# Optimization experiments

Measured on AMD Instinct MI355X. Metric: run time of the kernel, lower is better.

Reference implementation:

```python
import jax, jax.numpy as jnp
import numpy as np

H = W = 128
C = 256
NC = 15
BASE_SIZE = 8.0
SCALE = 4.0
RING = np.array([0, 1, 2, 5, 8, 7, 6, 3])  # clockwise ring of 3x3 kernel (row-major idx)
BIAS_CLS = float(-np.log((1.0 - 0.01) / 0.01))  # bias_init_with_prob(0.01)


def conv(x, w, b, pad):
    y = jax.lax.conv_general_dilated(x, w, (1, 1), [(pad, pad), (pad, pad)],
                                     dimension_numbers=('NCHW', 'OIHW', 'NCHW'))
    return y + b[None, :, None, None]


def conv_relu(x, w, b):
    return jax.nn.relu(conv(x, w, b, 1))


def gen_grid_anchors(h, w, stride):
    # AnchorGeneratorRotated: base anchor centered at 0.5*(base_size-1), shifted by stride grid
    ctr = 0.5 * (BASE_SIZE - 1.0)
    gx = jnp.arange(w, dtype=jnp.float32) * stride
    gy = jnp.arange(h, dtype=jnp.float32) * stride
    yy, xx = jnp.meshgrid(gy, gx, indexing='ij')  # row-major (y outer, x inner)
    size = BASE_SIZE * SCALE
    return jnp.stack([xx + ctr, yy + ctr,
                      jnp.full_like(xx, size), jnp.full_like(xx, size),
                      jnp.zeros_like(xx)], axis=-1).reshape(-1, 5)


def norm_angle(a):
    PI = np.pi
    return ((a + PI / 4.0) % PI) - PI / 4.0  # into [-pi/4, 3pi/4)


def rboxes_decode(anchors, deltas, wh_ratio_clip=1e-6):
    # anchors [HW,5], deltas [N,HW,5] -> [N,HW,5]
    max_ratio = float(np.abs(np.log(wh_ratio_clip)))
    dx, dy, dw, dh, dt = [deltas[..., i] for i in range(5)]
    dw = jnp.clip(dw, -max_ratio, max_ratio)
    dh = jnp.clip(dh, -max_ratio, max_ratio)
    ax, ay, aw, ah, aa = [anchors[..., i] for i in range(5)]
    cos, sin = jnp.cos(aa), jnp.sin(aa)
    gx = dx * aw * cos - dy * ah * sin + ax
    gy = dx * aw * sin + dy * ah * cos + ay
    gw = aw * jnp.exp(dw)
    gh = ah * jnp.exp(dh)
    ga = norm_angle(aa + dt)
    return jnp.stack([gx, gy, gw, gh, ga], axis=-1)


def bilinear_sample(x, ys, xs):
    # x [N,C,H,W]; ys/xs [N,H,W,K] float pixel coords -> [N,C,H,W,K], zero outside
    N, Cc, h, w = x.shape
    K = ys.shape[-1]
    x0 = jnp.floor(xs)
    y0 = jnp.floor(ys)
    wx1 = xs - x0
    wx0 = 1.0 - wx1
    wy1 = ys - y0
    wy0 = 1.0 - wy1
    xf = x.reshape(N, Cc, h * w)

    def gather(yi, wy, xi, wxx):
        valid = (yi >= 0) & (yi < h) & (xi >= 0) & (xi < w)
        yc = jnp.clip(yi, 0, h - 1).astype(jnp.int32)
        xc = jnp.clip(xi, 0, w - 1).astype(jnp.int32)
        idx = (yc * w + xc).reshape(N, -1)  # [N,H*W*K]
        v = jax.vmap(lambda xi_, ii_: jnp.take(xi_, ii_, axis=1))(xf, idx)
        v = v.reshape(N, Cc, h, w, K)
        wgt = jnp.where(valid, wy * wxx, 0.0)[:, None]  # [N,1,H,W,K]
        return v * wgt

    out = gather(y0, wy0, x0, wx0)
    out = out + gather(y0, wy0, x0 + 1.0, wx1)
    out = out + gather(y0 + 1.0, wy1, x0, wx0)
    out = out + gather(y0 + 1.0, wy1, x0 + 1.0, wx1)
    return out


def align_conv(x, refine_anchor, stride, w, b):
    # deformable 3x3 conv; sampling grid from refined rotated anchors
    N, Cc, h, ww = x.shape
    k = 3
    idx = jnp.arange(-1, 2, dtype=x.dtype)
    yy, xx = jnp.meshgrid(idx, idx, indexing='ij')
    xx = xx.reshape(-1)
    yy = yy.reshape(-1)  # [9] kernel offsets, row-major matching OIHW flatten
    axc, ayc, aw, ah, aa = [refine_anchor[..., i] for i in range(5)]
    s = jnp.asarray(stride, x.dtype)
    axc, ayc, aw, ah = axc / s, ayc / s, aw / s, ah / s
    cos, sin = jnp.cos(aa), jnp.sin(aa)
    dx = (aw / k)[..., None] * xx  # [N,h,w,9]
    dy = (ah / k)[..., None] * yy
    xs = cos[..., None] * dx - sin[..., None] * dy + axc[..., None]
    ys = sin[..., None] * dx + cos[..., None] * dy + ayc[..., None]
    sampled = bilinear_sample(x, ys, xs)  # [N,C,h,w,9]
    out = jnp.einsum('nchwk,ock->nohw', sampled, w.reshape(w.shape[0], Cc, 9))
    return jax.nn.relu(out + b[None, :, None, None])


def or_conv(x, w, b):
    # ORConv2d(256->32, arf_config=(1,8)): 8 spatially-rotated copies of each 3x3 filter
    o, ci = w.shape[0], w.shape[1]
    wf = w.reshape(o, ci, 9)
    rotated = []
    for r in range(8):
        src = np.arange(9)
        for j in range(8):
            src[RING[j]] = RING[(j - r) % 8]  # rotate ring by r*45deg, center fixed
        rotated.append(wf[..., src])
    wr = jnp.stack(rotated, axis=1).reshape(o * 8, ci, 3, 3)  # channel = o*8 + r
    br = jnp.repeat(b, 8)
    return conv(x, wr, br, 1)


def setup_inputs() -> dict:
    key = jax.random.key(0)
    ks = iter(jax.random.split(key, 32))
    d = {}
    d['feats'] = jax.random.normal(next(ks), (1, C, H, W), dtype=jnp.float32)
    def wlike(shape):
        return 0.01 * jax.random.normal(next(ks), shape, dtype=jnp.float32)
    d['fam_reg_w0'] = wlike((C, C, 3, 3)); d['fam_reg_b0'] = jnp.zeros((C,), jnp.float32)
    d['fam_reg_w1'] = wlike((C, C, 3, 3)); d['fam_reg_b1'] = jnp.zeros((C,), jnp.float32)
    d['fam_reg_hw'] = wlike((5, C, 1, 1)); d['fam_reg_hb'] = jnp.zeros((5,), jnp.float32)
    d['fam_cls_w0'] = wlike((C, C, 3, 3)); d['fam_cls_b0'] = jnp.zeros((C,), jnp.float32)
    d['fam_cls_w1'] = wlike((C, C, 3, 3)); d['fam_cls_b1'] = jnp.zeros((C,), jnp.float32)
    d['fam_cls_hw'] = wlike((NC, C, 1, 1)); d['fam_cls_hb'] = jnp.full((NC,), BIAS_CLS, jnp.float32)
    d['align_w'] = wlike((C, C, 3, 3)); d['align_b'] = jnp.zeros((C,), jnp.float32)
    d['or_w'] = wlike((C // 8, C, 3, 3)); d['or_b'] = jnp.zeros((C // 8,), jnp.float32)
    d['odm_reg_w0'] = wlike((C, C, 3, 3)); d['odm_reg_b0'] = jnp.zeros((C,), jnp.float32)
    d['odm_reg_w1'] = wlike((C, C, 3, 3)); d['odm_reg_b1'] = jnp.zeros((C,), jnp.float32)
    d['odm_reg_hw'] = wlike((5, C, 3, 3)); d['odm_reg_hb'] = jnp.zeros((5,), jnp.float32)
    d['odm_cls_w0'] = wlike((C, C // 8, 3, 3)); d['odm_cls_b0'] = jnp.zeros((C,), jnp.float32)
    d['odm_cls_w1'] = wlike((C, C, 3, 3)); d['odm_cls_b1'] = jnp.zeros((C,), jnp.float32)
    d['odm_cls_hw'] = wlike((NC, C, 3, 3)); d['odm_cls_hb'] = jnp.full((NC,), BIAS_CLS, jnp.float32)
    d['stride'] = 8
    return d


def reference(feats, fam_reg_w0, fam_reg_b0, fam_reg_w1, fam_reg_b1, fam_reg_hw, fam_reg_hb,
              fam_cls_w0, fam_cls_b0, fam_cls_w1, fam_cls_b1, fam_cls_hw, fam_cls_hb,
              align_w, align_b, or_w, or_b,
              odm_reg_w0, odm_reg_b0, odm_reg_w1, odm_reg_b1, odm_reg_hw, odm_reg_hb,
              odm_cls_w0, odm_cls_b0, odm_cls_w1, odm_cls_b1, odm_cls_hw, odm_cls_hb,
              stride):
    x = feats
    t = conv_relu(conv_relu(x, fam_reg_w0, fam_reg_b0), fam_reg_w1, fam_reg_b1)
    fam_bbox_pred = conv(t, fam_reg_hw, fam_reg_hb, 0)  # [N,5,h,w]
    t = conv_relu(conv_relu(x, fam_cls_w0, fam_cls_b0), fam_cls_w1, fam_cls_b1)
    fam_cls_pred = conv(t, fam_cls_hw, fam_cls_hb, 0)   # [N,NC,h,w]
    N, _, h, w = fam_bbox_pred.shape
    anchors = gen_grid_anchors(h, w, stride)  # [h*w,5]
    deltas = jax.lax.stop_gradient(fam_bbox_pred).transpose(0, 2, 3, 1).reshape(N, -1, 5)
    refine_anchor = rboxes_decode(anchors, deltas).reshape(N, h, w, 5)
    al = align_conv(x, refine_anchor, stride, align_w, align_b)  # [N,256,h,w]
    orf = or_conv(al, or_w, or_b)                                # [N,256,h,w]
    pooled = orf.reshape(N, -1, 8, h, w).max(axis=2)             # rotation-invariant pooling -> [N,32,h,w]
    t = conv_relu(conv_relu(pooled, odm_cls_w0, odm_cls_b0), odm_cls_w1, odm_cls_b1)
    odm_cls_pred = conv(t, odm_cls_hw, odm_cls_hb, 1)
    t = conv_relu(conv_relu(orf, odm_reg_w0, odm_reg_b0), odm_reg_w1, odm_reg_b1)
    odm_bbox_pred = conv(t, odm_reg_hw, odm_reg_hb, 1)
    return (fam_cls_pred, fam_bbox_pred, odm_cls_pred, odm_bbox_pred, anchors, refine_anchor)
```

## Files before the change

### kernel.cpp

```cpp
#include <hip/hip_runtime.h>
#include <hip/hip_bf16.h>
#include <hip/hip_fp16.h>

#define HW 128
#define NPX 16384
#define CC 256

typedef short  bf16x8  __attribute__((ext_vector_type(8)));
typedef short  short4v __attribute__((ext_vector_type(4)));
typedef float  f32x4   __attribute__((ext_vector_type(4)));
typedef unsigned int u32x4 __attribute__((ext_vector_type(4)));

static __device__ __forceinline__ short f2bs(float v) {
    union { float f; unsigned u; } x; x.f = v;
    unsigned r = x.u + 0x7FFFu + ((x.u >> 16) & 1u);
    return (short)(r >> 16);
}
static __device__ __forceinline__ float bs2f(short s) {
    union { unsigned u; float f; } x; x.u = ((unsigned)(unsigned short)s) << 16;
    return x.f;
}

static __device__ __forceinline__ int bx_swz() {
    return ((blockIdx.x & 7) << 5) | (blockIdx.x >> 3);
}

struct F8 { unsigned char b; };
__device__ __forceinline__ unsigned char enc8(float v) {
    unsigned short u = __half_as_ushort(__float2half(v));
    unsigned short s = u & 0x8000, mag = u & 0x7FFF;
    mag = (unsigned short)(mag + 0x0080);
    return (unsigned char)((unsigned short)(s | mag) >> 8);
}
__device__ __forceinline__ float dec8(F8 v) {
    return __half2float(__ushort_as_half((unsigned short)(v.b) << 8));
}
__device__ __forceinline__ float ldg_(const float* p) { return *p; }
__device__ __forceinline__ float ldg_(const F8* p)    { return dec8(*p); }

__constant__ int c_ROT9[8][9] = {
    {0,1,2,3,4,5,6,7,8},
    {3,0,1,6,4,2,7,8,5},
    {6,3,0,7,4,1,8,5,2},
    {7,6,3,8,4,0,5,2,1},
    {8,7,6,5,4,3,2,1,0},
    {5,8,7,2,4,6,1,0,3},
    {2,5,8,1,4,7,0,3,6},
    {1,2,5,0,4,8,3,6,7},
};

__device__ __forceinline__ void v9_decode_px(
    const float* bbox, int px, float s,
    float& gx, float& gy, float& gw, float& gh, float& ga)
{
    int y = px >> 7, x = px & 127;
    float ax = x * s + 3.5f, ay = y * s + 3.5f;
    float dx = bbox[0 * NPX + px];
    float dy = bbox[1 * NPX + px];
    float dw = bbox[2 * NPX + px];
    float dh = bbox[3 * NPX + px];
    float dt = bbox[4 * NPX + px];
    const float maxr = 13.815510558f;
    dw = fminf(fmaxf(dw, -maxr), maxr);
    dh = fminf(fmaxf(dh, -maxr), maxr);
    gx = dx * 32.f + ax;
    gy = dy * 32.f + ay;
    gw = 32.f * expf(dw);
    gh = 32.f * expf(dh);
    const float PI = 3.14159265358979323846f;
    float m = fmodf(dt + PI * 0.25f, PI);
    if (m < 0.f) m += PI;
    ga = m - PI * 0.25f;
}


__global__ __launch_bounds__(256) void v10_transpose(
    const float* __restrict__ f, short* __restrict__ xt)
{
    __shared__ float tile[32][33];
    int px0 = blockIdx.x * 32, ci0 = blockIdx.y * 32;
    int tx = threadIdx.x & 31, ty = threadIdx.x >> 5;
#pragma unroll
    for (int i = 0; i < 4; ++i) {
        int ci = ty + i * 8;
        tile[ci][tx] = f[(size_t)(ci0 + ci) * NPX + px0 + tx];
    }
    __syncthreads();
#pragma unroll
    for (int i = 0; i < 4; ++i) {
        int pxr = ty + i * 8;
        xt[(size_t)(px0 + pxr) * 256 + ci0 + tx] = f2bs(tile[tx][pxr]);
    }
}

__global__ __launch_bounds__(256) void v10_prep(
    const float* __restrict__ w, const float* __restrict__ bias,
    short* __restrict__ wb, float* __restrict__ bb,
    int Cout, int Cin, int OCP, int mode)
{
    int g = blockIdx.x * 256 + threadIdx.x;
    if (g < OCP) bb[g] = (g < Cout) ? ((mode == 1) ? bias[g >> 3] : bias[g]) : 0.f;
    int tot = 9 * OCP * Cin;
    if (g >= tot) return;
    int t   = g / (OCP * Cin);
    int rem = g - t * OCP * Cin;
    int oc  = rem / Cin;
    int ci  = rem - oc * Cin;
    float v = 0.f;
    if (oc < Cout) {
        if (mode == 0)      v = w[((size_t)oc * Cin + ci) * 9 + t];
        else if (mode == 1) { int o = oc >> 3, r = oc & 7;
                              v = w[((size_t)o * Cin + ci) * 9 + c_ROT9[r][t]]; }
        else if (t == 4)    v = w[(size_t)oc * Cin + ci];
    }
    wb[g] = f2bs(v);
}

__constant__ int c_JOB[14][5] = {
    {0,       256, 256, 256, 0},
    {589824,  256, 256, 256, 0},
    {1179648, 256, 256, 256, 0},
    {1769472, 256, 256, 256, 0},
    {2359296, 256, 256, 256, 0},
    {2949120, 256, 256, 256, 1},
    {3538944, 256, 256, 256, 0},
    {4128768, 256, 256, 256, 0},
    {4718592, 256, 256, 256, 0},
    {5308416, 5,   256, 64,  2},
    {5455872, 15,  256, 64,  2},
    {5603328, 5,   256, 64,  0},
    {5750784, 15,  256, 64,  0},
    {5898240, 256, 32,  256, 0},
};

__global__ __launch_bounds__(256) void v12_prepall(
    const float* w0, const float* w1, const float* w2, const float* w3,
    const float* w4, const float* w5, const float* w6, const float* w7,
    const float* w8, const float* w9, const float* w10, const float* w11,
    const float* w12, const float* w13,
    const float* b0, const float* b1, const float* b2, const float* b3,
    const float* b4, const float* b5, const float* b6, const float* b7,
    const float* b8, const float* b9, const float* b10, const float* b11,
    const float* b12, const float* b13,
    short* __restrict__ wball, float* __restrict__ bball)
{
    const float* ws_[14] = {w0,w1,w2,w3,w4,w5,w6,w7,w8,w9,w10,w11,w12,w13};
    const float* bs_[14] = {b0,b1,b2,b3,b4,b5,b6,b7,b8,b9,b10,b11,b12,b13};
    const int j = blockIdx.y;
    const int dst  = c_JOB[j][0];
    const int Cout = c_JOB[j][1];
    const int Cin  = c_JOB[j][2];
    const int OCP  = c_JOB[j][3];
    const int mode = c_JOB[j][4];
    const float* w = ws_[j];
    const float* bias = bs_[j];
    int g = blockIdx.x * 256 + threadIdx.x;
    if (g < OCP) bball[j * 256 + g] = (g < Cout) ? ((mode == 1) ? bias[g >> 3] : bias[g]) : 0.f;
    int tot = 9 * OCP * Cin;
    if (g >= tot) return;
    int t   = g / (OCP * Cin);
    int rem = g - t * OCP * Cin;
    int oc  = rem / Cin;
    int ci  = rem - oc * Cin;
    float v = 0.f;
    if (oc < Cout) {
        if (mode == 0)      v = w[((size_t)oc * Cin + ci) * 9 + t];
        else if (mode == 1) { int o = oc >> 3, r = oc & 7;
                              v = w[((size_t)o * Cin + ci) * 9 + c_ROT9[r][t]]; }
        else if (t == 4)    v = w[(size_t)oc * Cin + ci];
    }
    wball[dst + g] = f2bs(v);
}

template <int RELU, int HEAD, int ONLY1, int CIN, int OCG>
__device__ __forceinline__ void conv_body(
    short* S,
    const short* __restrict__ xin, const short* __restrict__ wb,
    const float* __restrict__ bb, void* __restrict__ outv,
    int CoutAct, int OCP, int bx, int oy)
{
    const int y    = bx >> 1;
    const int xh   = (bx & 1) * 64;
    const int ocb  = oy * 64 * OCG;
    const int tid  = threadIdx.x;
    const int wv   = tid >> 6;
    const int lane = tid & 63;
    const int quad = lane >> 4;
    const int l15  = lane & 15;
    const int ocw  = ocb + wv * 16 * OCG;

    int gofs[4], lofs[4];
#pragma unroll
    for (int i = 0; i < 4; ++i) {
        int e = tid + i * 256;
        gofs[i] = -1; lofs[i] = -1;
        if (e < 792) {
            int pos = e >> 2, part = e & 3;
            int r = pos / 66, c = pos - r * 66;
            int yy = y - 1 + r, xx = xh - 1 + c;
            lofs[i] = (r * 66 + c) * 40 + part * 8;
            if (yy >= 0 && yy < HW && xx >= 0 && xx < HW)
                gofs[i] = (yy * HW + xx) * CIN + part * 8;
        }
    }
    const bf16x8 zf = (bf16x8){0, 0, 0, 0, 0, 0, 0, 0};

    f32x4 acc[4][OCG];
#pragma unroll
    for (int p = 0; p < 4; ++p)
#pragma unroll
        for (int g = 0; g < OCG; ++g) acc[p][g] = (f32x4){0.f, 0.f, 0.f, 0.f};

    {
        bf16x8 st[4];
#pragma unroll
        for (int i = 0; i < 4; ++i) {
            st[i] = zf;
            if (gofs[i] >= 0) st[i] = *(const bf16x8*)(xin + gofs[i]);
        }
#pragma unroll
        for (int i = 0; i < 4; ++i)
            if (lofs[i] >= 0) *(bf16x8*)(&S[lofs[i]]) = st[i];
    }
    bf16x8 a[9][OCG];
#pragma unroll
    for (int t = (ONLY1 ? 4 : 0); t < (ONLY1 ? 5 : 9); ++t)
#pragma unroll
        for (int g = 0; g < OCG; ++g)
            a[t][g] = *(const bf16x8*)(wb +
                ((size_t)(t * OCP + ocw + g * 16 + l15) * CIN + quad * 8));
    __syncthreads();

    const int NST = CIN / 32;
    int cur = 0;
    for (int s = 0; s < NST; ++s) {
        const int cib = s * 32;

        bf16x8 st[4];
        if (s + 1 < NST) {
#pragma unroll
            for (int i = 0; i < 4; ++i) {
                st[i] = zf;
                if (gofs[i] >= 0)
                    st[i] = *(const bf16x8*)(xin + gofs[i] + cib + 32);
            }
        }

#pragma unroll
        for (int t = (ONLY1 ? 4 : 0); t < (ONLY1 ? 5 : 9); ++t) {
            const int r = t / 3, dxk = t % 3 - 1;
#pragma unroll
            for (int p = 0; p < 4; ++p) {
                int c = 1 + p * 16 + l15 + dxk;
                bf16x8 b = *(const bf16x8*)(&S[cur * 7920 + (r * 66 + c) * 40 + quad * 8]);
#pragma unroll
                for (int g = 0; g < OCG; ++g)
                    acc[p][g] = __builtin_amdgcn_mfma_f32_16x16x32_bf16(a[t][g], b, acc[p][g], 0, 0, 0);
            }
            if (s + 1 < NST) {
#pragma unroll
                for (int g = 0; g < OCG; ++g)
                    a[t][g] = *(const bf16x8*)(wb +
                        ((size_t)(t * OCP + ocw + g * 16 + l15) * CIN + cib + 32 + quad * 8));
            }
        }

        if (s + 1 < NST) {
#pragma unroll
            for (int i = 0; i < 4; ++i)
                if (lofs[i] >= 0) *(bf16x8*)(&S[(cur ^ 1) * 7920 + lofs[i]]) = st[i];
        }
        __syncthreads();
        cur ^= 1;
    }

#pragma unroll
    for (int p = 0; p < 4; ++p) {
        const int px = y * HW + xh + p * 16 + l15;
#pragma unroll
        for (int g = 0; g < OCG; ++g) {
            const int ocq = ocw + g * 16 + quad * 4;
            if (HEAD) {
                float* o = (float*)outv;
#pragma unroll
                for (int r = 0; r < 4; ++r)
                    if (ocq + r < CoutAct)
                        o[(size_t)(ocq + r) * NPX + px] = acc[p][g][r] + bb[ocq + r];
            } else {
                short4v s4;
#pragma unroll
                for (int r = 0; r < 4; ++r) {
                    float v = acc[p][g][r] + bb[ocq + r];
                    if (RELU) v = fmaxf(v, 0.f);
                    s4[r] = f2bs(v);
                }
                *(short4v*)((short*)outv + (size_t)px * 256 + ocq) = s4;
            }
        }
    }
}

template <int RELU, int HEAD, int ONLY1, int CIN, int OCG>
__global__ __launch_bounds__(256) void v13_conv(
    const short* __restrict__ xin, const short* __restrict__ wb,
    const float* __restrict__ bb, void* __restrict__ outv,
    int CoutAct, int OCP)
{
    __shared__ short S[2 * 7920];
    conv_body<RELU, HEAD, ONLY1, CIN, OCG>(S, xin, wb, bb, outv,
                                           CoutAct, OCP, bx_swz(), blockIdx.y);
}

template <int RELU, int HEAD, int ONLY1, int CIN0, int CIN1, int OCG, int NY, int OCP>
__global__ __launch_bounds__(256) void v13_pair(
    const short* __restrict__ in0, const short* __restrict__ in1,
    const short* __restrict__ wb0, const short* __restrict__ wb1,
    const float* __restrict__ bb0, const float* __restrict__ bb1,
    void* __restrict__ out0, void* __restrict__ out1,
    int cout0, int cout1)
{
    __shared__ short S[2 * 7920];
    const int ybr = blockIdx.y;
    if (ybr < NY)
        conv_body<RELU, HEAD, ONLY1, CIN0, OCG>(S, in0, wb0, bb0, out0,
                                                cout0, OCP, bx_swz(), ybr);
    else
        conv_body<RELU, HEAD, ONLY1, CIN1, OCG>(S, in1, wb1, bb1, out1,
                                                cout1, OCP, bx_swz(), ybr - NY);
}

__global__ __launch_bounds__(256) void v13_align(
    const short* __restrict__ xt, const float* __restrict__ bbox,
    const short* __restrict__ wb, const float* __restrict__ bb,
    const int* __restrict__ stride_p, short* __restrict__ outa)
{
    const int bx   = bx_swz();
    const int y    = bx >> 1;
    const int xh   = (bx & 1) * 64;
    const int ocb  = blockIdx.y * 128;
    const int tid  = threadIdx.x;
    const int wv   = tid >> 6, lane = tid & 63, quad = lane >> 4, l15 = lane & 15;
    const int ocw  = ocb + wv * 32;

    __shared__ int   s_idx[4][576];
    __shared__ float s_wgt[4][576];
    __shared__ short S[2][64 * 40];

    const float s = (float)(*stride_p);
    for (int e = tid; e < 576; e += 256) {
        int t = e >> 6, xi = e & 63;
        int px = y * HW + xh + xi;
        float gx, gy, gw, gh, ga;
        v9_decode_px(bbox, px, s, gx, gy, gw, gh, ga);
        float axc = gx / s, ayc = gy / s;
        float aw3 = gw / (3.f * s), ah3 = gh / (3.f * s);
        float cs = cosf(ga), sn = sinf(ga);
        float kx = (float)(t % 3 - 1), ky = (float)(t / 3 - 1);
        float ddx = aw3 * kx, ddy = ah3 * ky;
        float xf = cs * ddx - sn * ddy + axc;
        float yf = sn * ddx + cs * ddy + ayc;
        float fx = floorf(xf), fy = floorf(yf);
        int ix = (int)fx, iy = (int)fy;
        float wx1 = xf - fx, wx0 = 1.f - wx1;
        float wy1 = yf - fy, wy0 = 1.f - wy1;
        bool x0v = (ix >= 0) && (ix < HW), x1v = (ix + 1 >= 0) && (ix + 1 < HW);
        bool y0v = (iy >= 0) && (iy < HW), y1v = (iy + 1 >= 0) && (iy + 1 < HW);
        int x0c = min(max(ix, 0), HW - 1), x1c = min(max(ix + 1, 0), HW - 1);
        int y0c = min(max(iy, 0), HW - 1), y1c = min(max(iy + 1, 0), HW - 1);
        s_idx[0][e] = y0c * HW + x0c;
        s_idx[1][e] = y0c * HW + x1c;
        s_idx[2][e] = y1c * HW + x0c;
        s_idx[3][e] = y1c * HW + x1c;
        s_wgt[0][e] = (y0v && x0v) ? wy0 * wx0 : 0.f;
        s_wgt[1][e] = (y0v && x1v) ? wy0 * wx1 : 0.f;
        s_wgt[2][e] = (y1v && x0v) ? wy1 * wx0 : 0.f;
        s_wgt[3][e] = (y1v && x1v) ? wy1 * wx1 : 0.f;
    }

    f32x4 acc[4][2];
#pragma unroll
    for (int p = 0; p < 4; ++p) { acc[p][0] = (f32x4){0,0,0,0}; acc[p][1] = (f32x4){0,0,0,0}; }

    const int spx = tid >> 2;
    const int sq  = tid & 3;
    const int sw  = spx * 40 + sq * 8;
    const bf16x8 zf = (bf16x8){0, 0, 0, 0, 0, 0, 0, 0};

    __syncthreads();

    bf16x8 aC0, aC1;
    bf16x8 gN0, gN1, gN2, gN3;
    float  wN0, wN1, wN2, wN3;
    {
        int e = spx;
        int i0 = s_idx[0][e], i1 = s_idx[1][e], i2 = s_idx[2][e], i3 = s_idx[3][e];
        float w0 = s_wgt[0][e], w1 = s_wgt[1][e], w2 = s_wgt[2][e], w3 = s_wgt[3][e];
        const short* base = xt + sq * 8;
        bf16x8 g0 = *(const bf16x8*)(base + (size_t)i0 * 256);
        bf16x8 g1 = *(const bf16x8*)(base + (size_t)i1 * 256);
        bf16x8 g2 = *(const bf16x8*)(base + (size_t)i2 * 256);
        bf16x8 g3 = *(const bf16x8*)(base + (size_t)i3 * 256);
        float v[8];
#pragma unroll
        for (int i = 0; i < 8; ++i)
            v[i] = w0 * bs2f(g0[i]) + w1 * bs2f(g1[i]) + w2 * bs2f(g2[i]) + w3 * bs2f(g3[i]);
        u32x4 r;
#pragma unroll
        for (int i = 0; i < 4; ++i)
            asm("v_cvt_pk_bf16_f32 %0, %1, %2" : "=v"(r[i]) : "v"(v[2 * i]), "v"(v[2 * i + 1]));
        *(u32x4*)(&S[0][sw]) = r;
    }
    {
        int e = 64 + spx;
        int i0 = s_idx[0][e], i1 = s_idx[1][e], i2 = s_idx[2][e], i3 = s_idx[3][e];
        wN0 = s_wgt[0][e]; wN1 = s_wgt[1][e]; wN2 = s_wgt[2][e]; wN3 = s_wgt[3][e];
        const short* base = xt + sq * 8;
        gN0 = *(const bf16x8*)(base + (size_t)i0 * 256);
        gN1 = *(const bf16x8*)(base + (size_t)i1 * 256);
        gN2 = *(const bf16x8*)(base + (size_t)i2 * 256);
        gN3 = *(const bf16x8*)(base + (size_t)i3 * 256);
    }
    aC0 = *(const bf16x8*)(wb + ((size_t)(ocw + l15) * 256 + quad * 8));
    aC1 = *(const bf16x8*)(wb + ((size_t)(ocw + 16 + l15) * 256 + quad * 8));
    __syncthreads();

    int cur = 0;
    for (int cib = 0; cib < 256; cib += 32) {
        for (int t = 0; t < 9; ++t) {
            const bool have1 = !(cib == 224 && t == 8);
            const bool have2 = !(cib == 224 && t >= 7);
            const int t1 = (t == 8) ? 0 : t + 1;
            const int c1 = (t == 8) ? cib + 32 : cib;
            int t2 = t + 2, c2 = cib;
            if (t2 > 8) { t2 -= 9; c2 += 32; }

            bf16x8 gF0 = zf, gF1 = zf, gF2 = zf, gF3 = zf;
            float  wF0 = 0.f, wF1 = 0.f, wF2 = 0.f, wF3 = 0.f;
            if (have2) {
                int e = t2 * 64 + spx;
                int i0 = s_idx[0][e], i1 = s_idx[1][e], i2 = s_idx[2][e], i3 = s_idx[3][e];
                wF0 = s_wgt[0][e]; wF1 = s_wgt[1][e]; wF2 = s_wgt[2][e]; wF3 = s_wgt[3][e];
                const short* base = xt + c2 + sq * 8;
                gF0 = *(const bf16x8*)(base + (size_t)i0 * 256);
                gF1 = *(const bf16x8*)(base + (size_t)i1 * 256);
                gF2 = *(const bf16x8*)(base + (size_t)i2 * 256);
                gF3 = *(const bf16x8*)(base + (size_t)i3 * 256);
            }
            bf16x8 aN0 = aC0, aN1 = aC1;
            if (have1) {
                aN0 = *(const bf16x8*)(wb + ((size_t)(t1 * 256 + ocw + l15) * 256 + c1 + quad * 8));
                aN1 = *(const bf16x8*)(wb + ((size_t)(t1 * 256 + ocw + 16 + l15) * 256 + c1 + quad * 8));
            }

#pragma unroll
            for (int p = 0; p < 4; ++p) {
                bf16x8 b = *(const bf16x8*)(&S[cur][(p * 16 + l15) * 40 + quad * 8]);
                acc[p][0] = __builtin_amdgcn_mfma_f32_16x16x32_bf16(aC0, b, acc[p][0], 0, 0, 0);
                acc[p][1] = __builtin_amdgcn_mfma_f32_16x16x32_bf16(aC1, b, acc[p][1], 0, 0, 0);
            }

            if (have1) {
                float v[8];
#pragma unroll
                for (int i = 0; i < 8; ++i)
                    v[i] = wN0 * bs2f(gN0[i]) + wN1 * bs2f(gN1[i])
                         + wN2 * bs2f(gN2[i]) + wN3 * bs2f(gN3[i]);
                u32x4 r;
#pragma unroll
                for (int i = 0; i < 4; ++i)
                    asm("v_cvt_pk_bf16_f32 %0, %1, %2" : "=v"(r[i]) : "v"(v[2 * i]), "v"(v[2 * i + 1]));
                *(u32x4*)(&S[cur ^ 1][sw]) = r;
            }
            gN0 = gF0; gN1 = gF1; gN2 = gF2; gN3 = gF3;
            wN0 = wF0; wN1 = wF1; wN2 = wF2; wN3 = wF3;
            aC0 = aN0; aC1 = aN1;
            cur ^= 1;
            __syncthreads();
        }
    }

#pragma unroll
    for (int p = 0; p < 4; ++p) {
        const int px = y * HW + xh + p * 16 + l15;
#pragma unroll
        for (int g = 0; g < 2; ++g) {
            const int ocq = ocw + g * 16 + quad * 4;
            short4v s4;
#pragma unroll
            for (int r = 0; r < 4; ++r)
                s4[r] = f2bs(fmaxf(acc[p][g][r] + bb[ocq + r], 0.f));
            *(short4v*)(outa + (size_t)px * 256 + ocq) = s4;
        }
    }
}

__global__ __launch_bounds__(256) void v10_pool(
    const short* __restrict__ t1, short* __restrict__ p)
{
    int g = blockIdx.x * 256 + threadIdx.x;
    if (g >= 32 * NPX) return;
    int px = g >> 5, c = g & 31;
    const short* q = t1 + (size_t)px * 256 + c * 8;
    float m = bs2f(q[0]);
#pragma unroll
    for (int r = 1; r < 8; ++r) m = fmaxf(m, bs2f(q[r]));
    p[(size_t)px * 32 + c] = f2bs(m);
}

__global__ __launch_bounds__(256) void v9_decode(
    const float* __restrict__ bbox, float* __restrict__ anchors_out,
    float* __restrict__ refine_out, const int* __restrict__ stride_p)
{
    int px = blockIdx.x * 256 + threadIdx.x;
    if (px >= NPX) return;
    float s = (float)(*stride_p);
    int y = px >> 7, x = px & 127;
    anchors_out[px * 5 + 0] = x * s + 3.5f;
    anchors_out[px * 5 + 1] = y * s + 3.5f;
    anchors_out[px * 5 + 2] = 32.f;
    anchors_out[px * 5 + 3] = 32.f;
    anchors_out[px * 5 + 4] = 0.f;
    float gx, gy, gw, gh, ga;
    v9_decode_px(bbox, px, s, gx, gy, gw, gh, ga);
    refine_out[px * 5 + 0] = gx;
    refine_out[px * 5 + 1] = gy;
    refine_out[px * 5 + 2] = gw;
    refine_out[px * 5 + 3] = gh;
    refine_out[px * 5 + 4] = ga;
}

template <typename TIN, int RELU, int ORCONV>
__global__ __launch_bounds__(256) void v9_conv3x3(
    const TIN* __restrict__ in, const float* __restrict__ w,
    const float* __restrict__ bias, F8* __restrict__ out, int Cin)
{
    const int y   = blockIdx.x;
    const int ocb = blockIdx.y * 64;
    const int tid = threadIdx.x;
    const int xg  = tid & 15;
    const int og  = tid >> 4;
    const int x0  = xg * 8;
    const int oc0 = ocb + og * 4;

    __shared__ float srow[3][132];
    float acc[4][8];
#pragma unroll
    for (int i = 0; i < 4; ++i)
#pragma unroll
        for (int j = 0; j < 8; ++j) acc[i][j] = 0.f;

    for (int ci = 0; ci < Cin; ++ci) {
        __syncthreads();
        const TIN* inp = in + (size_t)ci * NPX;
        for (int t = tid; t < 3 * 130; t += 256) {
            int r = t / 130, c = t - r * 130;
            int yy = y - 1 + r, xx = c - 1;
            float v = 0.f;
            if (yy >= 0 && yy < HW && xx >= 0 && xx < HW) v = ldg_(inp + yy * HW + xx);
            srow[r][c] = v;
        }
        __syncthreads();
        float wv[4][9];
#pragma unroll
        for (int i = 0; i < 4; ++i) {
            if (ORCONV) {
                int oc = oc0 + i;
                const float* wp = w + ((size_t)(oc >> 3) * Cin + ci) * 9;
                const int* rot = c_ROT9[oc & 7];
#pragma unroll
                for (int k = 0; k < 9; ++k) wv[i][k] = wp[rot[k]];
            } else {
                const float* wp = w + ((size_t)(oc0 + i) * Cin + ci) * 9;
#pragma unroll
                for (int k = 0; k < 9; ++k) wv[i][k] = wp[k];
            }
        }
#pragma unroll
        for (int r = 0; r < 3; ++r) {
            float iv[10];
#pragma unroll
            for (int c = 0; c < 10; ++c) iv[c] = srow[r][x0 + c];
#pragma unroll
            for (int dxk = 0; dxk < 3; ++dxk)
#pragma unroll
                for (int i = 0; i < 4; ++i)
#pragma unroll
                    for (int j = 0; j < 8; ++j)
                        acc[i][j] += iv[j + dxk] * wv[i][r * 3 + dxk];
        }
    }
#pragma unroll
    for (int i = 0; i < 4; ++i) {
        float b = ORCONV ? bias[(oc0 + i) >> 3] : bias[oc0 + i];
#pragma unroll
        for (int j = 0; j < 8; ++j) {
            float v = acc[i][j] + b;
            if (RELU) v = fmaxf(v, 0.f);
            out[(size_t)(oc0 + i) * NPX + y * HW + x0 + j].b = enc8(v);
        }
    }
}

__global__ __launch_bounds__(256) void v9_head1x1(
    const F8* __restrict__ in, const float* __restrict__ w,
    const float* __restrict__ bias, float* __restrict__ out, int Cout)
{
    int g = blockIdx.x * 256 + threadIdx.x;
    if (g >= Cout * NPX) return;
    int px = g & (NPX - 1);
    int oc = g >> 14;
    float acc = bias[oc];
    const float* wp = w + (size_t)oc * CC;
    for (int ci = 0; ci < CC; ++ci)
        acc += dec8(in[(size_t)ci * NPX + px]) * wp[ci];
    out[g] = acc;
}

__global__ __launch_bounds__(256) void v9_head3x3(
    const F8* __restrict__ in, const float* __restrict__ w,
    const float* __restrict__ bias, float* __restrict__ out, int Cout)
{
    int g = blockIdx.x * 256 + threadIdx.x;
    if (g >= Cout * NPX) return;
    int px = g & (NPX - 1);
    int oc = g >> 14;
    int y = px >> 7, x = px & 127;
    float acc = bias[oc];
    for (int ci = 0; ci < CC; ++ci) {
        const F8* ip = in + (size_t)ci * NPX;
        const float* wp = w + ((size_t)oc * CC + ci) * 9;
#pragma unroll
        for (int dy = 0; dy < 3; ++dy) {
            int yy = y + dy - 1;
            if (yy < 0 || yy >= HW) continue;
#pragma unroll
            for (int dxk = 0; dxk < 3; ++dxk) {
                int xx = x + dxk - 1;
                if (xx < 0 || xx >= HW) continue;
                acc += dec8(ip[yy * HW + xx]) * wp[dy * 3 + dxk];
            }
        }
    }
    out[g] = acc;
}

__global__ __launch_bounds__(256) void v9_align(
    const float* __restrict__ in, const float* __restrict__ bbox,
    const float* __restrict__ w, const float* __restrict__ bias,
    const int* __restrict__ stride_p, F8* __restrict__ out)
{
    const int y   = blockIdx.x;
    const int ocb = blockIdx.y * 64;
    const int tid = threadIdx.x;
    const int xg  = tid & 15;
    const int og  = tid >> 4;
    const int x0  = xg * 8;
    const int oc0 = ocb + og * 4;

    __shared__ float smp[9][128];
    __shared__ int   s_ix[1152], s_iy[1152];
    __shared__ float s_wx1[1152], s_wy1[1152];

    const float s = (float)(*stride_p);
    for (int t = tid; t < 1152; t += 256) {
        int k = t >> 7, xx = t & 127;
        int px = y * HW + xx;
        float gx, gy, gw, gh, ga;
        v9_decode_px(bbox, px, s, gx, gy, gw, gh, ga);
        float axc = gx / s, ayc = gy / s;
        float aw3 = gw / (s * 3.f), ah3 = gh / (s * 3.f);
        float cs = cosf(ga), sn = sinf(ga);
        float kx = (float)(k % 3 - 1), ky = (float)(k / 3 - 1);
        float ddx = aw3 * kx, ddy = ah3 * ky;
        float xf = cs * ddx - sn * ddy + axc;
        float yf = sn * ddx + cs * ddy + ayc;
        float fx = floorf(xf), fy = floorf(yf);
        s_ix[t]  = (int)fx;
        s_iy[t]  = (int)fy;
        s_wx1[t] = xf - fx;
        s_wy1[t] = yf - fy;
    }

    float acc[4][8];
#pragma unroll
    for (int i = 0; i < 4; ++i)
#pragma unroll
        for (int j = 0; j < 8; ++j) acc[i][j] = 0.f;

    for (int ci = 0; ci < CC; ++ci) {
        __syncthreads();
        const float* ip = in + (size_t)ci * NPX;
        for (int t = tid; t < 1152; t += 256) {
            int ix = s_ix[t], iy = s_iy[t];
            float wx1 = s_wx1[t], wx0 = 1.f - wx1;
            float wy1 = s_wy1[t], wy0 = 1.f - wy1;
            float v = 0.f;
            bool xv0 = (ix >= 0) && (ix < HW);
            bool xv1 = (ix + 1 >= 0) && (ix + 1 < HW);
            bool yv0 = (iy >= 0) && (iy < HW);
            bool yv1 = (iy + 1 >= 0) && (iy + 1 < HW);
            if (yv0 && xv0) v += ip[iy * HW + ix] * wy0 * wx0;
            if (yv0 && xv1) v += ip[iy * HW + ix + 1] * wy0 * wx1;
            if (yv1 && xv0) v += ip[(iy + 1) * HW + ix] * wy1 * wx0;
            if (yv1 && xv1) v += ip[(iy + 1) * HW + ix + 1] * wy1 * wx1;
            smp[t >> 7][t & 127] = v;
        }
        __syncthreads();

        float wv[4][9];
#pragma unroll
        for (int i = 0; i < 4; ++i) {
            const float* wp = w + ((size_t)(oc0 + i) * CC + ci) * 9;
#pragma unroll
            for (int k = 0; k < 9; ++k) wv[i][k] = wp[k];
        }
#pragma unroll
        for (int k = 0; k < 9; ++k) {
            float iv[8];
#pragma unroll
            for (int j = 0; j < 8; ++j) iv[j] = smp[k][x0 + j];
#pragma unroll
            for (int i = 0; i < 4; ++i)
#pragma unroll
                for (int j = 0; j < 8; ++j)
                    acc[i][j] += iv[j] * wv[i][k];
        }
    }
#pragma unroll
    for (int i = 0; i < 4; ++i) {
        float b = bias[oc0 + i];
#pragma unroll
        for (int j = 0; j < 8; ++j)
            out[(size_t)(oc0 + i) * NPX + y * HW + x0 + j].b =
                enc8(fmaxf(acc[i][j] + b, 0.f));
    }
}

__global__ __launch_bounds__(256) void v9_pool(
    const F8* __restrict__ orf, F8* __restrict__ pooled)
{
    int g = blockIdx.x * 256 + threadIdx.x;
    if (g >= 32 * NPX) return;
    int px = g & (NPX - 1);
    int c  = g >> 14;
    float m = -3.4e38f;
#pragma unroll
    for (int r = 0; r < 8; ++r)
        m = fmaxf(m, dec8(orf[(size_t)(c * 8 + r) * NPX + px]));
    pooled[g].b = enc8(m);
}

extern "C" void kernel_launch(void* const* d_in, const int* in_sizes, int n_in,
                              void* d_out, int out_size, void* d_ws, size_t ws_size,
                              hipStream_t stream)
{
    const float* feats = (const float*)d_in[0];
    const float* frw0 = (const float*)d_in[1];  const float* frb0 = (const float*)d_in[2];
    const float* frw1 = (const float*)d_in[3];  const float* frb1 = (const float*)d_in[4];
    const float* frhw = (const float*)d_in[5];  const float* frhb = (const float*)d_in[6];
    const float* fcw0 = (const float*)d_in[7];  const float* fcb0 = (const float*)d_in[8];
    const float* fcw1 = (const float*)d_in[9];  const float* fcb1 = (const float*)d_in[10];
    const float* fchw = (const float*)d_in[11]; const float* fchb = (const float*)d_in[12];
    const float* alw  = (const float*)d_in[13]; const float* alb  = (const float*)d_in[14];
    const float* orw  = (const float*)d_in[15]; const float* orb  = (const float*)d_in[16];
    const float* drw0 = (const float*)d_in[17]; const float* drb0 = (const float*)d_in[18];
    const float* drw1 = (const float*)d_in[19]; const float* drb1 = (const float*)d_in[20];
    const float* drhw = (const float*)d_in[21]; const float* drhb = (const float*)d_in[22];
    const float* dcw0 = (const float*)d_in[23]; const float* dcb0 = (const float*)d_in[24];
    const float* dcw1 = (const float*)d_in[25]; const float* dcb1 = (const float*)d_in[26];
    const float* dchw = (const float*)d_in[27]; const float* dchb = (const float*)d_in[28];
    const int*  stride_p = (const int*)d_in[29];

    float* out = (float*)d_out;
    float* o_fam_cls  = out;
    float* o_fam_bbox = out + 245760;
    float* o_odm_cls  = out + 327680;
    float* o_odm_bbox = out + 573440;
    float* o_anchors  = out + 655360;
    float* o_refine   = out + 737280;

    dim3 blk(256);

    const size_t NEED3     = 55097344;
    const size_t NEED2     = 38172672;
    const size_t NEED_FAST = 27395072;
    const size_t NEED_V9   = 8912896;

    if (ws_size >= NEED3) {
        char* ws = (char*)d_ws;
        short* xt = (short*)(ws + 0);
        short* T0 = (short*)(ws + 8388608);
        short* T1 = (short*)(ws + 16777216);
        short* T2 = (short*)(ws + 25165824);
        short* T3 = (short*)(ws + 33554432);
        short* P  = (short*)(ws + 41943040);
        short* WA = (short*)(ws + 42991616);
        float* BA = (float*)(ws + 55083008);

        v12_prepall<<<dim3(2304, 14), blk, 0, stream>>>(
            frw0, frw1, fcw0, fcw1, alw, orw, drw0, drw1, dcw1,
            frhw, fchw, drhw, dchw, dcw0,
            frb0, frb1, fcb0, fcb1, alb, orb, drb0, drb1, dcb1,
            frhb, fchb, drhb, dchb, dcb0,
            WA, BA);
        v10_transpose<<<dim3(512, 8), blk, 0, stream>>>(feats, xt);

        v13_pair<1, 0, 0, 256, 256, 2, 2, 256><<<dim3(256, 4), blk, 0, stream>>>(
            xt, xt, WA + 0, WA + 1179648, BA + 0 * 256, BA + 2 * 256, T0, T2, 256, 256);
        v13_pair<1, 0, 0, 256, 256, 2, 2, 256><<<dim3(256, 4), blk, 0, stream>>>(
            T0, T2, WA + 589824, WA + 1769472, BA + 1 * 256, BA + 3 * 256, T1, T3, 256, 256);
        v13_pair<0, 1, 1, 256, 256, 1, 1, 64><<<dim3(256, 2), blk, 0, stream>>>(
            T1, T3, WA + 5308416, WA + 5455872, BA + 9 * 256, BA + 10 * 256,
            o_fam_bbox, o_fam_cls, 5, 15);
        v9_decode<<<dim3(64), blk, 0, stream>>>(o_fam_bbox, o_anchors, o_refine, stride_p);
        v13_align<<<dim3(256, 2), blk, 0, stream>>>(xt, o_fam_bbox, WA + 2359296, BA + 4 * 256, stride_p, T0);
        v13_conv<0, 0, 0, 256, 2><<<dim3(256, 2), blk, 0, stream>>>(T0, WA + 2949120, BA + 5 * 256, T1, 256, 256);
        v10_pool<<<dim3(2048), blk, 0, stream>>>(T1, P);
        v13_pair<1, 0, 0, 256, 32, 2, 2, 256><<<dim3(256, 4), blk, 0, stream>>>(
            T1, P, WA + 3538944, WA + 5898240, BA + 6 * 256, BA + 13 * 256, T0, T2, 256, 256);
        v13_pair<1, 0, 0, 256, 256, 2, 2, 256><<<dim3(256, 4), blk, 0, stream>>>(
            T0, T2, WA + 4128768, WA + 4718592, BA + 7 * 256, BA + 8 * 256, T1, T3, 256, 256);
        v13_pair<0, 1, 0, 256, 256, 1, 1, 64><<<dim3(256, 2), blk, 0, stream>>>(
            T1, T3, WA + 5603328, WA + 5750784, BA + 11 * 256, BA + 12 * 256,
            o_odm_bbox, o_odm_cls, 5, 15);
    } else if (ws_size >= NEED2) {
        char* ws = (char*)d_ws;
        short* xt = (short*)(ws + 0);
        short* T0 = (short*)(ws + 8388608);
        short* T1 = (short*)(ws + 16777216);
        short* P  = (short*)(ws + 25165824);
        short* WA = (short*)(ws + 26214400);
        float* BA = (float*)(ws + 38158336);

        dim3 gc(256, 2), gh(256, 1);

        v12_prepall<<<dim3(2304, 14), blk, 0, stream>>>(
            frw0, frw1, fcw0, fcw1, alw, orw, drw0, drw1, dcw1,
            frhw, fchw, drhw, dchw, dcw0,
            frb0, frb1, fcb0, fcb1, alb, orb, drb0, drb1, dcb1,
            frhb, fchb, drhb, dchb, dcb0,
            WA, BA);
        v10_transpose<<<dim3(512, 8), blk, 0, stream>>>(feats, xt);

        v13_conv<1, 0, 0, 256, 2><<<gc, blk, 0, stream>>>(xt, WA + 0,       BA + 0 * 256, T0, 256, 256);
        v13_conv<1, 0, 0, 256, 2><<<gc, blk, 0, stream>>>(T0, WA + 589824,  BA + 1 * 256, T1, 256, 256);
        v13_conv<0, 1, 1, 256, 1><<<gh, blk, 0, stream>>>(T1, WA + 5308416, BA + 9 * 256, o_fam_bbox, 5, 64);
        v13_conv<1, 0, 0, 256, 2><<<gc, blk, 0, stream>>>(xt, WA + 1179648, BA + 2 * 256, T0, 256, 256);
        v13_conv<1, 0, 0, 256, 2><<<gc, blk, 0, stream>>>(T0, WA + 1769472, BA + 3 * 256, T1, 256, 256);
        v13_conv<0, 1, 1, 256, 1><<<gh, blk, 0, stream>>>(T1, WA + 5455872, BA + 10 * 256, o_fam_cls, 15, 64);
        v9_decode<<<dim3(64), blk, 0, stream>>>(o_fam_bbox, o_anchors, o_refine, stride_p);
        v13_align<<<dim3(256, 2), blk, 0, stream>>>(xt, o_fam_bbox, WA + 2359296, BA + 4 * 256, stride_p, T0);
        v13_conv<0, 0, 0, 256, 2><<<gc, blk, 0, stream>>>(T0, WA + 2949120, BA + 5 * 256, T1, 256, 256);
        v10_pool<<<dim3(2048), blk, 0, stream>>>(T1, P);
        v13_conv<1, 0, 0, 256, 2><<<gc, blk, 0, stream>>>(T1, WA + 3538944, BA + 6 * 256, T0, 256, 256);
        v13_conv<1, 0, 0, 256, 2><<<gc, blk, 0, stream>>>(T0, WA + 4128768, BA + 7 * 256, T1, 256, 256);
        v13_conv<0, 1, 0, 256, 1><<<gh, blk, 0, stream>>>(T1, WA + 5603328, BA + 11 * 256, o_odm_bbox, 5, 64);
        v13_conv<1, 0, 0, 32, 2><<<gc, blk, 0, stream>>>(P, WA + 5898240, BA + 13 * 256, T0, 256, 256);
        v13_conv<1, 0, 0, 256, 2><<<gc, blk, 0, stream>>>(T0, WA + 4718592, BA + 8 * 256, T1, 256, 256);
        v13_conv<0, 1, 0, 256, 1><<<gh, blk, 0, stream>>>(T1, WA + 5750784, BA + 12 * 256, o_odm_cls, 15, 64);
    } else if (ws_size >= NEED_FAST) {
        char* ws = (char*)d_ws;
        short* xt = (short*)(ws + 0);
        short* T0 = (short*)(ws + 8388608);
        short* T1 = (short*)(ws + 16777216);
        short* P  = (short*)(ws + 25165824);
        short* WB = (short*)(ws + 26214400);
        float* BB = (float*)(ws + 27394048);

        dim3 gc(256, 2), gh(256, 1);

        v10_transpose<<<dim3(512, 8), blk, 0, stream>>>(feats, xt);

#define PREP(W, B, COUT, CIN, OCP, MODE) \
        v10_prep<<<dim3((9 * (OCP) * (CIN) + 255) / 256), blk, 0, stream>>>( \
            W, B, WB, BB, COUT, CIN, OCP, MODE)

        PREP(frw0, frb0, 256, 256, 256, 0);
        v13_conv<1, 0, 0, 256, 2><<<gc, blk, 0, stream>>>(xt, WB, BB, T0, 256, 256);
        PREP(frw1, frb1, 256, 256, 256, 0);
        v13_conv<1, 0, 0, 256, 2><<<gc, blk, 0, stream>>>(T0, WB, BB, T1, 256, 256);
        PREP(frhw, frhb, 5, 256, 64, 2);
        v13_conv<0, 1, 1, 256, 1><<<gh, blk, 0, stream>>>(T1, WB, BB, o_fam_bbox, 5, 64);
        PREP(fcw0, fcb0, 256, 256, 256, 0);
        v13_conv<1, 0, 0, 256, 2><<<gc, blk, 0, stream>>>(xt, WB, BB, T0, 256, 256);
        PREP(fcw1, fcb1, 256, 256, 256, 0);
        v13_conv<1, 0, 0, 256, 2><<<gc, blk, 0, stream>>>(T0, WB, BB, T1, 256, 256);
        PREP(fchw, fchb, 15, 256, 64, 2);
        v13_conv<0, 1, 1, 256, 1><<<gh, blk, 0, stream>>>(T1, WB, BB, o_fam_cls, 15, 64);
        v9_decode<<<dim3(64), blk, 0, stream>>>(o_fam_bbox, o_anchors, o_refine, stride_p);
        PREP(alw, alb, 256, 256, 256, 0);
        v13_align<<<dim3(256, 2), blk, 0, stream>>>(xt, o_fam_bbox, WB, BB, stride_p, T0);
        PREP(orw, orb, 256, 256, 256, 1);
        v13_conv<0, 0, 0, 256, 2><<<gc, blk, 0, stream>>>(T0, WB, BB, T1, 256, 256);
        v10_pool<<<dim3(2048), blk, 0, stream>>>(T1, P);
        PREP(drw0, drb0, 256, 256, 256, 0);
        v13_conv<1, 0, 0, 256, 2><<<gc, blk, 0, stream>>>(T1, WB, BB, T0, 256, 256);
        PREP(drw1, drb1, 256, 256, 256, 0);
        v13_conv<1, 0, 0, 256, 2><<<gc, blk, 0, stream>>>(T0, WB, BB, T1, 256, 256);
        PREP(drhw, drhb, 5, 256, 64, 0);
        v13_conv<0, 1, 0, 256, 1><<<gh, blk, 0, stream>>>(T1, WB, BB, o_odm_bbox, 5, 64);
        PREP(dcw0, dcb0, 256, 32, 256, 0);
        v13_conv<1, 0, 0, 32, 2><<<gc, blk, 0, stream>>>(P, WB, BB, T0, 256, 256);
        PREP(dcw1, dcb1, 256, 256, 256, 0);
        v13_conv<1, 0, 0, 256, 2><<<gc, blk, 0, stream>>>(T0, WB, BB, T1, 256, 256);
        PREP(dchw, dchb, 15, 256, 64, 0);
        v13_conv<0, 1, 0, 256, 1><<<gh, blk, 0, stream>>>(T1, WB, BB, o_odm_cls, 15, 64);
#undef PREP
    } else if (ws_size >= NEED_V9) {
        F8* A = (F8*)d_ws;
        F8* B = (F8*)((char*)d_ws + 4194304);
        F8* P = (F8*)((char*)d_ws + 8388608);
        dim3 gconv(128, 4);

        v9_conv3x3<float, 1, 0><<<gconv, blk, 0, stream>>>(feats, frw0, frb0, A, 256);
        v9_conv3x3<F8,    1, 0><<<gconv, blk, 0, stream>>>(A, frw1, frb1, B, 256);
        v9_head1x1<<<dim3(5 * 64), blk, 0, stream>>>(B, frhw, frhb, o_fam_bbox, 5);
        v9_conv3x3<float, 1, 0><<<gconv, blk, 0, stream>>>(feats, fcw0, fcb0, A, 256);
        v9_conv3x3<F8,    1, 0><<<gconv, blk, 0, stream>>>(A, fcw1, fcb1, B, 256);
        v9_head1x1<<<dim3(15 * 64), blk, 0, stream>>>(B, fchw, fchb, o_fam_cls, 15);
        v9_decode<<<dim3(64), blk, 0, stream>>>(o_fam_bbox, o_anchors, o_refine, stride_p);
        v9_align<<<gconv, blk, 0, stream>>>(feats, o_fam_bbox, alw, alb, stride_p, A);
        v9_conv3x3<F8, 0, 1><<<gconv, blk, 0, stream>>>(A, orw, orb, B, 256);
        v9_pool<<<dim3(2048), blk, 0, stream>>>(B, P);
        v9_conv3x3<F8, 1, 0><<<gconv, blk, 0, stream>>>(B, drw0, drb0, A, 256);
        v9_conv3x3<F8, 1, 0><<<gconv, blk, 0, stream>>>(A, drw1, drb1, B, 256);
        v9_head3x3<<<dim3(5 * 64), blk, 0, stream>>>(B, drhw, drhb, o_odm_bbox, 5);
        v9_conv3x3<F8, 1, 0><<<gconv, blk, 0, stream>>>(P, dcw0, dcb0, A, 32);
        v9_conv3x3<F8, 1, 0><<<gconv, blk, 0, stream>>>(A, dcw1, dcb1, B, 256);
        v9_head3x3<<<dim3(15 * 64), blk, 0, stream>>>(B, dchw, dchb, o_odm_cls, 15);
    }
}
```

Before: 551.1 us.

## Widen 3x3 conv tiles to all 256 output channels per block

Adds a new conv body where each block computes all 256 output channels (64 per wave, 4x4 MFMA accumulator tiles) for a 64-pixel row segment, instead of splitting output channels across two grid-y blocks. This halves the number of blocks and reuses each staged input tile from LDS across twice as many output channels, cutting redundant input loads. Weight fragments for the next tap are prefetched into registers while the current tap runs, and occupancy is pinned at 2 waves per EU. The trade-off is higher register pressure and a smaller grid of 512 blocks, which may under-fill the GPU.

```diff
diff --git a/kernel.cpp b/kernel.cpp
--- a/kernel.cpp
+++ b/kernel.cpp
@@ -300,6 +300,128 @@
     }
 }
 
+template <int RELU, int CIN>
+__device__ __forceinline__ void conv_body4(
+    short* S,
+    const short* __restrict__ xin, const short* __restrict__ wb,
+    const float* __restrict__ bb, short* __restrict__ outb, int bx)
+{
+    const int y    = bx >> 1;
+    const int xh   = (bx & 1) * 64;
+    const int tid  = threadIdx.x;
+    const int wv   = tid >> 6;
+    const int lane = tid & 63;
+    const int quad = lane >> 4;
+    const int l15  = lane & 15;
+    const int ocw  = wv * 64;
+
+    int gofs[4], lofs[4];
+#pragma unroll
+    for (int i = 0; i < 4; ++i) {
+        int e = tid + i * 256;
+        gofs[i] = -1; lofs[i] = -1;
+        if (e < 792) {
+            int pos = e >> 2, part = e & 3;
+            int r = pos / 66, c = pos - r * 66;
+            int yy = y - 1 + r, xx = xh - 1 + c;
+            lofs[i] = (r * 66 + c) * 40 + part * 8;
+            if (yy >= 0 && yy < HW && xx >= 0 && xx < HW)
+                gofs[i] = (yy * HW + xx) * CIN + part * 8;
+        }
+    }
+    const bf16x8 zf = (bf16x8){0, 0, 0, 0, 0, 0, 0, 0};
+
+    f32x4 acc[4][4];
+#pragma unroll
+    for (int p = 0; p < 4; ++p)
+#pragma unroll
+        for (int g = 0; g < 4; ++g) acc[p][g] = (f32x4){0.f, 0.f, 0.f, 0.f};
+
+    {
+        bf16x8 st[4];
+#pragma unroll
+        for (int i = 0; i < 4; ++i) {
+            st[i] = zf;
+            if (gofs[i] >= 0) st[i] = *(const bf16x8*)(xin + gofs[i]);
+        }
+#pragma unroll
+        for (int i = 0; i < 4; ++i)
+            if (lofs[i] >= 0) *(bf16x8*)(&S[lofs[i]]) = st[i];
+    }
+    bf16x8 aC[4], aN[4];
+#pragma unroll
+    for (int g = 0; g < 4; ++g)
+        aC[g] = *(const bf16x8*)(wb +
+            ((size_t)(ocw + g * 16 + l15) * CIN + quad * 8));
+#pragma unroll
+    for (int g = 0; g < 4; ++g) aN[g] = aC[g];
+    __syncthreads();
+
+    const int NST = CIN / 32;
+    int cur = 0;
+    for (int s = 0; s < NST; ++s) {
+        const int cib = s * 32;
+
+        bf16x8 st[4];
+        if (s + 1 < NST) {
+#pragma unroll
+            for (int i = 0; i < 4; ++i) {
+                st[i] = zf;
+                if (gofs[i] >= 0)
+                    st[i] = *(const bf16x8*)(xin + gofs[i] + cib + 32);
+            }
+        }
+
+#pragma unroll
+        for (int t = 0; t < 9; ++t) {
+            const int nt   = (t == 8) ? 0 : t + 1;
+            const int ncib = (t == 8) ? cib + 32 : cib;
+            if (!(s == NST - 1 && t == 8)) {
+#pragma unroll
+                for (int g = 0; g < 4; ++g)
+                    aN[g] = *(const bf16x8*)(wb +
+                        ((size_t)(nt * 256 + ocw + g * 16 + l15) * CIN + ncib + quad * 8));
+            }
+            const int r = t / 3, dxk = t % 3 - 1;
+#pragma unroll
+            for (int p = 0; p < 4; ++p) {
+                int c = 1 + p * 16 + l15 + dxk;
+                bf16x8 b = *(const bf16x8*)(&S[cur * 7920 + (r * 66 + c) * 40 + quad * 8]);
+#pragma unroll
+                for (int g = 0; g < 4; ++g)
+                    acc[p][g] = __builtin_amdgcn_mfma_f32_16x16x32_bf16(aC[g], b, acc[p][g], 0, 0, 0);
+            }
+#pragma unroll
+            for (int g = 0; g < 4; ++g) aC[g] = aN[g];
+        }
+
+        if (s + 1 < NST) {
+#pragma unroll
+            for (int i = 0; i < 4; ++i)
+                if (lofs[i] >= 0) *(bf16x8*)(&S[(cur ^ 1) * 7920 + lofs[i]]) = st[i];
+        }
+        __syncthreads();
+        cur ^= 1;
+    }
+
+#pragma unroll
+    for (int p = 0; p < 4; ++p) {
+        const int px = y * HW + xh + p * 16 + l15;
+#pragma unroll
+        for (int g = 0; g < 4; ++g) {
+            const int ocq = ocw + g * 16 + quad * 4;
+            short4v s4;
+#pragma unroll
+            for (int r = 0; r < 4; ++r) {
+                float v = acc[p][g][r] + bb[ocq + r];
+                if (RELU) v = fmaxf(v, 0.f);
+                s4[r] = f2bs(v);
+            }
+            *(short4v*)(outb + (size_t)px * 256 + ocq) = s4;
+        }
+    }
+}
+
 template <int RELU, int HEAD, int ONLY1, int CIN, int OCG>
 __global__ __launch_bounds__(256) void v13_conv(
     const short* __restrict__ xin, const short* __restrict__ wb,
@@ -327,6 +449,31 @@
     else
         conv_body<RELU, HEAD, ONLY1, CIN1, OCG>(S, in1, wb1, bb1, out1,
                                                 cout1, OCP, bx_swz(), ybr - NY);
+}
+
+template <int RELU, int CIN>
+__global__ __launch_bounds__(256) __attribute__((amdgpu_waves_per_eu(2, 2)))
+void v14_conv(
+    const short* __restrict__ xin, const short* __restrict__ wb,
+    const float* __restrict__ bb, short* __restrict__ outb)
+{
+    __shared__ short S[2 * 7920];
+    conv_body4<RELU, CIN>(S, xin, wb, bb, outb, bx_swz());
+}
+
+template <int RELU, int CIN0, int CIN1>
+__global__ __launch_bounds__(256) __attribute__((amdgpu_waves_per_eu(2, 2)))
+void v14_pair(
+    const short* __restrict__ in0, const short* __restrict__ in1,
+    const short* __restrict__ wb0, const short* __restrict__ wb1,
+    const float* __restrict__ bb0, const float* __restrict__ bb1,
+    short* __restrict__ out0, short* __restrict__ out1)
+{
+    __shared__ short S[2 * 7920];
+    if (blockIdx.y == 0)
+        conv_body4<RELU, CIN0>(S, in0, wb0, bb0, out0, bx_swz());
+    else
+        conv_body4<RELU, CIN1>(S, in1, wb1, bb1, out1, bx_swz());
 }
 
 __global__ __launch_bounds__(256) void v13_align(
@@ -805,21 +952,21 @@
             WA, BA);
         v10_transpose<<<dim3(512, 8), blk, 0, stream>>>(feats, xt);
 
-        v13_pair<1, 0, 0, 256, 256, 2, 2, 256><<<dim3(256, 4), blk, 0, stream>>>(
-            xt, xt, WA + 0, WA + 1179648, BA + 0 * 256, BA + 2 * 256, T0, T2, 256, 256);
-        v13_pair<1, 0, 0, 256, 256, 2, 2, 256><<<dim3(256, 4), blk, 0, stream>>>(
-            T0, T2, WA + 589824, WA + 1769472, BA + 1 * 256, BA + 3 * 256, T1, T3, 256, 256);
+        v14_pair<1, 256, 256><<<dim3(256, 2), blk, 0, stream>>>(
+            xt, xt, WA + 0, WA + 1179648, BA + 0 * 256, BA + 2 * 256, T0, T2);
+        v14_pair<1, 256, 256><<<dim3(256, 2), blk, 0, stream>>>(
+            T0, T2, WA + 589824, WA + 1769472, BA + 1 * 256, BA + 3 * 256, T1, T3);
         v13_pair<0, 1, 1, 256, 256, 1, 1, 64><<<dim3(256, 2), blk, 0, stream>>>(
             T1, T3, WA + 5308416, WA + 5455872, BA + 9 * 256, BA + 10 * 256,
             o_fam_bbox, o_fam_cls, 5, 15);
         v9_decode<<<dim3(64), blk, 0, stream>>>(o_fam_bbox, o_anchors, o_refine, stride_p);
         v13_align<<<dim3(256, 2), blk, 0, stream>>>(xt, o_fam_bbox, WA + 2359296, BA + 4 * 256, stride_p, T0);
-        v13_conv<0, 0, 0, 256, 2><<<dim3(256, 2), blk, 0, stream>>>(T0, WA + 2949120, BA + 5 * 256, T1, 256, 256);
+        v14_conv<0, 256><<<dim3(256, 1), blk, 0, stream>>>(T0, WA + 2949120, BA + 5 * 256, T1);
         v10_pool<<<dim3(2048), blk, 0, stream>>>(T1, P);
-        v13_pair<1, 0, 0, 256, 32, 2, 2, 256><<<dim3(256, 4), blk, 0, stream>>>(
-            T1, P, WA + 3538944, WA + 5898240, BA + 6 * 256, BA + 13 * 256, T0, T2, 256, 256);
-        v13_pair<1, 0, 0, 256, 256, 2, 2, 256><<<dim3(256, 4), blk, 0, stream>>>(
-            T0, T2, WA + 4128768, WA + 4718592, BA + 7 * 256, BA + 8 * 256, T1, T3, 256, 256);
+        v14_pair<1, 256, 32><<<dim3(256, 2), blk, 0, stream>>>(
+            T1, P, WA + 3538944, WA + 5898240, BA + 6 * 256, BA + 13 * 256, T0, T2);
+        v14_pair<1, 256, 256><<<dim3(256, 2), blk, 0, stream>>>(
+            T0, T2, WA + 4128768, WA + 4718592, BA + 7 * 256, BA + 8 * 256, T1, T3);
         v13_pair<0, 1, 0, 256, 256, 1, 1, 64><<<dim3(256, 2), blk, 0, stream>>>(
             T1, T3, WA + 5603328, WA + 5750784, BA + 11 * 256, BA + 12 * 256,
             o_odm_bbox, o_odm_cls, 5, 15);
```

Result: no change. 550.3 us (-0.1%).
